# Performance work log

Measured on AMD Instinct MI355X. Metric: run time of the kernel, lower is better.

Reference implementation:

```python
import jax, jax.numpy as jnp
import numpy as np

V, D, H, F, L, SMAX = 32000, 768, 12, 3072, 6, 512
DN = D // H
NEG = -1e9
EPS = 1e-5


def _pos_encoding(S, d, dtype):
    # pe[pos,2i]   = sin(pos / 10000**(2i/d))
    # pe[pos,2i+1] = cos(pos / 10000**(2(i+1)/d))   (note the i+1, as in source)
    pos = jnp.arange(S, dtype=jnp.float32)[:, None]
    i = jnp.arange(d // 2, dtype=jnp.float32)[None, :]
    pe_sin = jnp.sin(pos / jnp.power(10000.0, 2.0 * i / d))
    pe_cos = jnp.cos(pos / jnp.power(10000.0, 2.0 * (i + 1.0) / d))
    pe = jnp.zeros((S, d), jnp.float32)
    pe = pe.at[:, 0::2].set(pe_sin).at[:, 1::2].set(pe_cos)
    return pe.astype(dtype)


def _layernorm(z, g, b):
    m = jnp.mean(z, axis=-1, keepdims=True)
    v = jnp.mean(jnp.square(z - m), axis=-1, keepdims=True)
    return (z - m) * jax.lax.rsqrt(v + EPS) * g + b


def setup_inputs() -> dict:
    key = jax.random.key(0)
    ks = jax.random.split(key, 20)
    s = 0.02
    inp = {
        "x": jax.random.randint(ks[0], (16, 512), 0, V, dtype=jnp.int64 if jax.config.read("jax_enable_x64") else jnp.int32),
        "padding_mask": jax.random.randint(ks[1], (16, 512, 512), 0, 2, dtype=jnp.int32),
        "emb": jax.random.normal(ks[2], (V, D), jnp.float32) * s,
        # per-head separate projections, stacked: [L, H, D, DN]
        "Wq": jax.random.normal(ks[3], (L, H, D, DN), jnp.float32) * s,
        "bq": jnp.zeros((L, H, DN), jnp.float32),
        "Wk": jax.random.normal(ks[4], (L, H, D, DN), jnp.float32) * s,
        "bk": jnp.zeros((L, H, DN), jnp.float32),
        "Wv": jax.random.normal(ks[5], (L, H, D, DN), jnp.float32) * s,
        "bv": jnp.zeros((L, H, DN), jnp.float32),
        "Wo": jax.random.normal(ks[6], (L, D, D), jnp.float32) * s,
        "bo": jnp.zeros((L, D), jnp.float32),
        "W1": jax.random.normal(ks[7], (L, D, F), jnp.float32) * s,
        "b1": jnp.zeros((L, F), jnp.float32),
        "W2": jax.random.normal(ks[8], (L, F, D), jnp.float32) * s,
        "b2": jnp.zeros((L, D), jnp.float32),
        "g1": jnp.ones((L, D), jnp.float32),
        "be1": jnp.zeros((L, D), jnp.float32),
        "g2": jnp.ones((L, D), jnp.float32),
        "be2": jnp.zeros((L, D), jnp.float32),
    }
    return inp


def reference(x, padding_mask, emb, Wq, bq, Wk, bk, Wv, bv, Wo, bo,
              W1, b1, W2, b2, g1, be1, g2, be2):
    B, S = x.shape
    h = emb[x]                                   # [B,S,D]
    h = h + _pos_encoding(S, D, h.dtype)[None]   # dropout is identity in eval
    bias = padding_mask.astype(h.dtype)[:, None] * NEG   # [B,1,S,S]
    scale = 1.0 / np.sqrt(DN)
    for l in range(L):
        q = jnp.einsum("bsd,hde->bhse", h, Wq[l]) + bq[l][None, :, None, :]
        k = jnp.einsum("bsd,hde->bhse", h, Wk[l]) + bk[l][None, :, None, :]
        v = jnp.einsum("bsd,hde->bhse", h, Wv[l]) + bv[l][None, :, None, :]
        scores = jnp.einsum("bhse,bhte->bhst", q, k) * scale + bias
        attn = jax.nn.softmax(scores, axis=-1)
        o = jnp.einsum("bhst,bhte->bhse", attn, v)        # [B,H,S,DN]
        o = o.transpose(0, 2, 1, 3).reshape(B, S, D)      # concat heads
        o = o @ Wo[l] + bo[l]
        h = _layernorm(h + o, g1[l], be1[l])
        ff = jax.nn.relu(h @ W1[l] + b1[l]) @ W2[l] + b2[l]
        h = _layernorm(h + ff, g2[l], be2[l])
    return h
```

## Files before the change

### kernel.cpp

```cpp
#include <hip/hip_runtime.h>
#include <hip/hip_bf16.h>
#include <math.h>

#define B_  16
#define S_  512
#define D_  768
#define H_  12
#define DN_ 64
#define F_  3072
#define L_  6
#define T_  (B_*S_)
#define QKVN 2304
#define TDC ((size_t)T_*D_)

typedef unsigned short ushort_t;
typedef short short8 __attribute__((ext_vector_type(8)));
typedef float floatx4 __attribute__((ext_vector_type(4)));

#define LDS_AS(p) ((__attribute__((address_space(3))) void*)(p))
#define GLB_AS(p) ((const __attribute__((address_space(1))) void*)(p))

static __device__ __forceinline__ float b2f(ushort_t u) {
  union { unsigned int i; float f; } x; x.i = ((unsigned int)u) << 16; return x.f;
}
static __device__ __forceinline__ ushort_t f2b(float f) {
  union { float f; unsigned int i; } x; x.f = f;
  unsigned int r = x.i + 0x7fffu + ((x.i >> 16) & 1u);
  return (ushort_t)(r >> 16);
}

__global__ __launch_bounds__(64) void probe_x(const int* __restrict__ x,
                                              int* __restrict__ xstride) {
  if (threadIdx.x == 0) {
    int allzero = 1;
    for (int i = 0; i < 64; ++i) allzero &= (x[2 * i + 1] == 0) ? 1 : 0;
    *xstride = allzero ? 2 : 1;
  }
}

__global__ __launch_bounds__(256) void pe_kernel(float* __restrict__ pe) {
  const int s = blockIdx.x;
  const float pos = (float)s;
  for (int d = threadIdx.x; d < D_; d += 256) {
    float v;
    if ((d & 1) == 0) {
      float freq = powf(10000.0f, -(float)d * (1.0f / 768.0f));
      v = sinf(pos * freq);
    } else {
      float freq = powf(10000.0f, -(float)(d + 1) * (1.0f / 768.0f));
      v = cosf(pos * freq);
    }
    pe[(size_t)s * D_ + d] = v;
  }
}

__global__ __launch_bounds__(256) void embed_pe(const int* __restrict__ x,
                                                const int* __restrict__ xstride,
                                                const float* __restrict__ emb,
                                                const float* __restrict__ pe,
                                                float* __restrict__ h32,
                                                ushort_t* __restrict__ h16) {
  const int t = blockIdx.x;
  const int s = t & (S_ - 1);
  const int tok = x[t * (*xstride)];
  const float* ep = emb + (size_t)tok * D_;
  const float* pp = pe + (size_t)s * D_;
  for (int d = threadIdx.x; d < D_; d += 256) {
    float v = ep[d] + pp[d];
    h32[(size_t)t * D_ + d] = v;
    h16[(size_t)t * D_ + d] = f2b(v);
  }
}

__global__ __launch_bounds__(256) void mask_bias(const int* __restrict__ mask,
                                                 ushort_t* __restrict__ bias) {
  const size_t i = ((size_t)blockIdx.x * 256 + threadIdx.x) * 4;
  int4 m = *(const int4*)(mask + i);
  ushort4 o;
  o.x = m.x ? f2b(-1e9f) : (ushort_t)0;
  o.y = m.y ? f2b(-1e9f) : (ushort_t)0;
  o.z = m.z ? f2b(-1e9f) : (ushort_t)0;
  o.w = m.w ? f2b(-1e9f) : (ushort_t)0;
  *(ushort4*)(bias + i) = o;
}

__global__ __launch_bounds__(256) void pack_bias(const float* __restrict__ bq,
                                                 const float* __restrict__ bk,
                                                 const float* __restrict__ bv,
                                                 float* __restrict__ bqkv) {
  const int i = blockIdx.x * 256 + threadIdx.x;
  if (i < L_ * D_) {
    const int l = i / D_, c = i - l * D_;
    bqkv[(size_t)l * QKVN + c]          = bq[i];
    bqkv[(size_t)l * QKVN + 768 + c]    = bk[i];
    bqkv[(size_t)l * QKVN + 1536 + c]   = bv[i];
  }
}

__global__ __launch_bounds__(256) void transpose_cast(const float* __restrict__ in,
                                                      ushort_t* __restrict__ out,
                                                      int R, int C, int ZH,
                                                      size_t strideL, size_t strideH) {
  __shared__ float tb[32][33];
  const int c0 = blockIdx.x * 32, r0 = blockIdx.y * 32;
  const int z = blockIdx.z;
  const float* ib = in + (size_t)z * R * C;
  ushort_t* ob = out + (size_t)(z / ZH) * strideL + (size_t)(z % ZH) * strideH;
  const int i = threadIdx.x >> 5;
  const int j = threadIdx.x & 31;
  #pragma unroll
  for (int t = 0; t < 4; ++t)
    tb[i + 8 * t][j] = ib[(size_t)(r0 + i + 8 * t) * C + c0 + j];
  __syncthreads();
  #pragma unroll
  for (int t = 0; t < 4; ++t)
    ob[(size_t)(c0 + i + 8 * t) * R + r0 + j] = f2b(tb[j][i + 8 * t]);
}

__global__ __launch_bounds__(256) void transpose_v(const ushort_t* __restrict__ qkv,
                                                   ushort_t* __restrict__ vT) {
  __shared__ ushort_t tb[32][33];
  const int s0 = blockIdx.x * 32, e0 = blockIdx.y * 32;
  const int bh = blockIdx.z;
  const int b = bh / 12, hh = bh - b * 12;
  const int i = threadIdx.x >> 5, j = threadIdx.x & 31;
  #pragma unroll
  for (int t = 0; t < 4; ++t)
    tb[i + 8 * t][j] = qkv[((size_t)(b * S_ + s0 + i + 8 * t)) * QKVN + 1536 + hh * 64 + e0 + j];
  __syncthreads();
  #pragma unroll
  for (int t = 0; t < 4; ++t)
    vT[((size_t)(bh * 64 + e0 + i + 8 * t)) * S_ + s0 + j] = tb[j][i + 8 * t];
}

template<int RELU>
__global__ __launch_bounds__(256) void gemm_mfma(const ushort_t* __restrict__ A,
                                                 const ushort_t* __restrict__ Bt,
                                                 const float* __restrict__ bias,
                                                 ushort_t* __restrict__ C,
                                                 int N, int K) {
  __shared__ ushort_t Alds[128 * 32];
  __shared__ ushort_t Blds[128 * 32];
  const int tid = threadIdx.x;
  const int lane = tid & 63, wave = tid >> 6;
  const int l16 = lane & 15, quad = lane >> 4;
  const int m0 = (wave >> 1) * 64, n0 = (wave & 1) * 64;
  const int nb = gridDim.x;
  const int flat = blockIdx.y * nb + blockIdx.x;
  const int grp = flat / (8 * nb);
  const int rem = flat - grp * 8 * nb;
  const int bm = (grp * 8 + (rem & 7)) * 128;
  const int bn = (rem >> 3) * 128;
  const int r0 = tid >> 2, koff = (tid & 3) * 8;

  const ushort_t* ga0 = A  + (size_t)(bm + r0) * K + koff;
  const ushort_t* ga1 = ga0 + (size_t)64 * K;
  const ushort_t* gb0 = Bt + (size_t)(bn + r0) * K + koff;
  const ushort_t* gb1 = gb0 + (size_t)64 * K;
  ushort_t* la0 = &Alds[tid * 8];
  ushort_t* la1 = &Alds[64 * 32 + tid * 8];
  ushort_t* lb0 = &Blds[tid * 8];
  ushort_t* lb1 = &Blds[64 * 32 + tid * 8];

  floatx4 acc[4][4] = {};
  for (int k0 = 0; k0 < K; k0 += 32) {
    __syncthreads();
    __builtin_amdgcn_global_load_lds(GLB_AS(ga0 + k0), LDS_AS(la0), 16, 0, 0);
    __builtin_amdgcn_global_load_lds(GLB_AS(ga1 + k0), LDS_AS(la1), 16, 0, 0);
    __builtin_amdgcn_global_load_lds(GLB_AS(gb0 + k0), LDS_AS(lb0), 16, 0, 0);
    __builtin_amdgcn_global_load_lds(GLB_AS(gb1 + k0), LDS_AS(lb1), 16, 0, 0);
    __syncthreads();
    short8 af[4], bf[4];
    #pragma unroll
    for (int fi = 0; fi < 4; ++fi)
      af[fi] = *(const short8*)&Alds[(m0 + fi * 16 + l16) * 32 + quad * 8];
    #pragma unroll
    for (int fj = 0; fj < 4; ++fj)
      bf[fj] = *(const short8*)&Blds[(n0 + fj * 16 + l16) * 32 + quad * 8];
    #pragma unroll
    for (int fi = 0; fi < 4; ++fi)
      #pragma unroll
      for (int fj = 0; fj < 4; ++fj)
        acc[fi][fj] = __builtin_amdgcn_mfma_f32_16x16x32_bf16(af[fi], bf[fj], acc[fi][fj], 0, 0, 0);
  }
  #pragma unroll
  for (int fi = 0; fi < 4; ++fi) {
    #pragma unroll
    for (int fj = 0; fj < 4; ++fj) {
      const int row = bm + m0 + fi * 16 + quad * 4;
      const int col = bn + n0 + fj * 16 + l16;
      const float bv = bias[col];
      #pragma unroll
      for (int r = 0; r < 4; ++r) {
        float v = acc[fi][fj][r] + bv;
        if (RELU) v = fmaxf(v, 0.0f);
        C[(size_t)(row + r) * N + col] = f2b(v);
      }
    }
  }
}

__global__ __launch_bounds__(256) void gemm_mfma_sk(const ushort_t* __restrict__ A,
                                                    const ushort_t* __restrict__ Bt,
                                                    const float* __restrict__ bias,
                                                    ushort_t* __restrict__ P,
                                                    int N, int K) {
  __shared__ ushort_t Alds[128 * 32];
  __shared__ ushort_t Blds[128 * 32];
  const int tid = threadIdx.x;
  const int lane = tid & 63, wave = tid >> 6;
  const int l16 = lane & 15, quad = lane >> 4;
  const int m0 = (wave >> 1) * 64, n0 = (wave & 1) * 64;
  const int nb = gridDim.x;
  const int flat = blockIdx.y * nb + blockIdx.x;
  const int grp = flat / (8 * nb);
  const int rem = flat - grp * 8 * nb;
  const int bm = (grp * 8 + (rem & 7)) * 128;
  const int bn = (rem >> 3) * 128;
  const int r0 = tid >> 2, koff = (tid & 3) * 8;
  const int z = blockIdx.z;
  const int Kh = K >> 1;

  const ushort_t* ga0 = A  + (size_t)(bm + r0) * K + (size_t)z * Kh + koff;
  const ushort_t* ga1 = ga0 + (size_t)64 * K;
  const ushort_t* gb0 = Bt + (size_t)(bn + r0) * K + (size_t)z * Kh + koff;
  const ushort_t* gb1 = gb0 + (size_t)64 * K;
  ushort_t* la0 = &Alds[tid * 8];
  ushort_t* la1 = &Alds[64 * 32 + tid * 8];
  ushort_t* lb0 = &Blds[tid * 8];
  ushort_t* lb1 = &Blds[64 * 32 + tid * 8];
  ushort_t* Pz = P + (size_t)z * T_ * N;

  floatx4 acc[4][4] = {};
  for (int k0 = 0; k0 < Kh; k0 += 32) {
    __syncthreads();
    __builtin_amdgcn_global_load_lds(GLB_AS(ga0 + k0), LDS_AS(la0), 16, 0, 0);
    __builtin_amdgcn_global_load_lds(GLB_AS(ga1 + k0), LDS_AS(la1), 16, 0, 0);
    __builtin_amdgcn_global_load_lds(GLB_AS(gb0 + k0), LDS_AS(lb0), 16, 0, 0);
    __builtin_amdgcn_global_load_lds(GLB_AS(gb1 + k0), LDS_AS(lb1), 16, 0, 0);
    __syncthreads();
    short8 af[4], bf[4];
    #pragma unroll
    for (int fi = 0; fi < 4; ++fi)
      af[fi] = *(const short8*)&Alds[(m0 + fi * 16 + l16) * 32 + quad * 8];
    #pragma unroll
    for (int fj = 0; fj < 4; ++fj)
      bf[fj] = *(const short8*)&Blds[(n0 + fj * 16 + l16) * 32 + quad * 8];
    #pragma unroll
    for (int fi = 0; fi < 4; ++fi)
      #pragma unroll
      for (int fj = 0; fj < 4; ++fj)
        acc[fi][fj] = __builtin_amdgcn_mfma_f32_16x16x32_bf16(af[fi], bf[fj], acc[fi][fj], 0, 0, 0);
  }
  #pragma unroll
  for (int fi = 0; fi < 4; ++fi) {
    #pragma unroll
    for (int fj = 0; fj < 4; ++fj) {
      const int row = bm + m0 + fi * 16 + quad * 4;
      const int col = bn + n0 + fj * 16 + l16;
      const float bv = (z == 0) ? bias[col] : 0.0f;
      #pragma unroll
      for (int r = 0; r < 4; ++r) {
        float v = acc[fi][fj][r] + bv;
        Pz[(size_t)(row + r) * N + col] = f2b(v);
      }
    }
  }
}

__global__ __launch_bounds__(256) void attn_mfma(const ushort_t* __restrict__ qkv,
                                                 const ushort_t* __restrict__ vT,
                                                 const ushort_t* __restrict__ bias,
                                                 ushort_t* __restrict__ o) {
  __shared__ ushort_t Qs[64][72];
  __shared__ ushort_t Ks[64][72];
  __shared__ ushort_t Vt[64][72];
  __shared__ ushort_t Ps[64][72];
  const int qt = blockIdx.x, hh = blockIdx.y, b = blockIdx.z;
  const int tid = threadIdx.x;
  const int lane = tid & 63, w = tid >> 6;
  const int l16 = lane & 15, quad = lane >> 4;

  for (int c = tid; c < 1024; c += 256) {
    const int row = c >> 4, e0 = (c & 15) * 4;
    *(ushort4*)&Qs[row][e0] =
        *(const ushort4*)(qkv + ((size_t)(b * S_ + qt * 64 + row)) * QKVN + hh * 64 + e0);
  }

  floatx4 Oa[4] = {};
  float mrow[4] = {-3e38f, -3e38f, -3e38f, -3e38f};
  float lrow[4] = {};
  const ushort_t* vbase = vT + ((size_t)(b * H_ + hh) * 64) * S_;

  for (int kt = 0; kt < 8; ++kt) {
    __syncthreads();
    for (int c = tid; c < 1024; c += 256) {
      const int row = c >> 4, e0 = (c & 15) * 4;
      *(ushort4*)&Ks[row][e0] =
          *(const ushort4*)(qkv + ((size_t)(b * S_ + kt * 64 + row)) * QKVN + 768 + hh * 64 + e0);
      *(ushort4*)&Vt[row][e0] =
          *(const ushort4*)(vbase + (size_t)row * S_ + kt * 64 + e0);
    }
    __syncthreads();

    floatx4 sa[4] = {};
    #pragma unroll
    for (int st = 0; st < 2; ++st) {
      short8 aq = *(const short8*)&Qs[w * 16 + l16][st * 32 + quad * 8];
      #pragma unroll
      for (int fj = 0; fj < 4; ++fj) {
        short8 bk = *(const short8*)&Ks[fj * 16 + l16][st * 32 + quad * 8];
        sa[fj] = __builtin_amdgcn_mfma_f32_16x16x32_bf16(aq, bk, sa[fj], 0, 0, 0);
      }
    }

    #pragma unroll
    for (int r = 0; r < 4; ++r) {
      const int qrow = qt * 64 + w * 16 + quad * 4 + r;
      const ushort_t* bp = bias + ((size_t)b * S_ + qrow) * S_ + kt * 64 + l16;
      float s0 = sa[0][r] * 0.125f + b2f(bp[0]);
      float s1 = sa[1][r] * 0.125f + b2f(bp[16]);
      float s2 = sa[2][r] * 0.125f + b2f(bp[32]);
      float s3 = sa[3][r] * 0.125f + b2f(bp[48]);
      float mt = fmaxf(fmaxf(s0, s1), fmaxf(s2, s3));
      mt = fmaxf(mt, __shfl_xor(mt, 1)); mt = fmaxf(mt, __shfl_xor(mt, 2));
      mt = fmaxf(mt, __shfl_xor(mt, 4)); mt = fmaxf(mt, __shfl_xor(mt, 8));
      const float mn = fmaxf(mrow[r], mt);
      const float alpha = __expf(mrow[r] - mn);
      mrow[r] = mn;
      float p0 = __expf(s0 - mn), p1 = __expf(s1 - mn);
      float p2 = __expf(s2 - mn), p3 = __expf(s3 - mn);
      const int prow = w * 16 + quad * 4 + r;
      Ps[prow][ 0 + l16] = f2b(p0);
      Ps[prow][16 + l16] = f2b(p1);
      Ps[prow][32 + l16] = f2b(p2);
      Ps[prow][48 + l16] = f2b(p3);
      float rs = p0 + p1 + p2 + p3;
      rs += __shfl_xor(rs, 1); rs += __shfl_xor(rs, 2);
      rs += __shfl_xor(rs, 4); rs += __shfl_xor(rs, 8);
      lrow[r] = lrow[r] * alpha + rs;
      Oa[0][r] *= alpha; Oa[1][r] *= alpha; Oa[2][r] *= alpha; Oa[3][r] *= alpha;
    }

    #pragma unroll
    for (int st = 0; st < 2; ++st) {
      short8 ap = *(const short8*)&Ps[w * 16 + l16][st * 32 + quad * 8];
      #pragma unroll
      for (int fe = 0; fe < 4; ++fe) {
        short8 bv = *(const short8*)&Vt[fe * 16 + l16][st * 32 + quad * 8];
        Oa[fe] = __builtin_amdgcn_mfma_f32_16x16x32_bf16(ap, bv, Oa[fe], 0, 0, 0);
      }
    }
  }

  #pragma unroll
  for (int r = 0; r < 4; ++r) {
    const float inv = 1.0f / lrow[r];
    const size_t tok = (size_t)(b * S_ + qt * 64 + w * 16 + quad * 4 + r);
    #pragma unroll
    for (int fe = 0; fe < 4; ++fe)
      o[tok * D_ + hh * 64 + fe * 16 + l16] = f2b(Oa[fe][r] * inv);
  }
}

__global__ __launch_bounds__(256) void add_ln(float* __restrict__ h,
                                              const ushort_t* __restrict__ r,
                                              const float* __restrict__ g,
                                              const float* __restrict__ be,
                                              ushort_t* __restrict__ h16) {
  const int t = blockIdx.x;
  const int tid = threadIdx.x;
  __shared__ float red[8];
  const size_t base = (size_t)t * D_;
  float x0 = h[base + tid]       + b2f(r[base + tid])       + b2f(r[TDC + base + tid]);
  float x1 = h[base + tid + 256] + b2f(r[base + tid + 256]) + b2f(r[TDC + base + tid + 256]);
  float x2 = h[base + tid + 512] + b2f(r[base + tid + 512]) + b2f(r[TDC + base + tid + 512]);
  float s = x0 + x1 + x2;
  #pragma unroll
  for (int off = 32; off > 0; off >>= 1) s += __shfl_down(s, off);
  if ((tid & 63) == 0) red[tid >> 6] = s;
  __syncthreads();
  if (tid == 0) red[4] = (red[0] + red[1] + red[2] + red[3]) * (1.0f / 768.0f);
  __syncthreads();
  const float m = red[4];
  float d0 = x0 - m, d1 = x1 - m, d2 = x2 - m;
  float s2 = d0 * d0 + d1 * d1 + d2 * d2;
  #pragma unroll
  for (int off = 32; off > 0; off >>= 1) s2 += __shfl_down(s2, off);
  if ((tid & 63) == 0) red[tid >> 6] = s2;
  __syncthreads();
  if (tid == 0) red[5] = (red[0] + red[1] + red[2] + red[3]) * (1.0f / 768.0f);
  __syncthreads();
  const float rs = rsqrtf(red[5] + 1e-5f);
  float y0 = d0 * rs * g[tid]       + be[tid];
  float y1 = d1 * rs * g[tid + 256] + be[tid + 256];
  float y2 = d2 * rs * g[tid + 512] + be[tid + 512];
  h[base + tid]       = y0; h16[base + tid]       = f2b(y0);
  h[base + tid + 256] = y1; h16[base + tid + 256] = f2b(y1);
  h[base + tid + 512] = y2; h16[base + tid + 512] = f2b(y2);
}

__global__ __launch_bounds__(256) void write_out(const float* __restrict__ h,
                                                 float* __restrict__ out, int n) {
  int i = blockIdx.x * 256 + threadIdx.x;
  if (i < n) out[i] = h[i];
}

extern "C" void kernel_launch(void* const* d_in, const int* in_sizes, int n_in,
                              void* d_out, int out_size, void* d_ws, size_t ws_size,
                              hipStream_t stream) {
  (void)in_sizes; (void)n_in; (void)out_size; (void)ws_size;
  const int* x    = (const int*)d_in[0];
  const int* mask = (const int*)d_in[1];
  const float* emb = (const float*)d_in[2];
  const float* Wq  = (const float*)d_in[3];
  const float* bq  = (const float*)d_in[4];
  const float* Wk  = (const float*)d_in[5];
  const float* bk  = (const float*)d_in[6];
  const float* Wv  = (const float*)d_in[7];
  const float* bv  = (const float*)d_in[8];
  const float* Wo  = (const float*)d_in[9];
  const float* bo  = (const float*)d_in[10];
  const float* W1  = (const float*)d_in[11];
  const float* b1  = (const float*)d_in[12];
  const float* W2  = (const float*)d_in[13];
  const float* b2  = (const float*)d_in[14];
  const float* g1  = (const float*)d_in[15];
  const float* be1 = (const float*)d_in[16];
  const float* g2  = (const float*)d_in[17];
  const float* be2 = (const float*)d_in[18];

  const size_t TD  = TDC;
  const size_t DD  = (size_t)D_ * D_;
  const size_t WDD = (size_t)L_ * DD;
  const size_t WDF = (size_t)L_ * D_ * F_;

  float* h32 = (float*)d_ws;
  ushort_t* h16  = (ushort_t*)(h32 + TD);
  ushort_t* qkv16 = h16 + TD;
  ushort_t* o1   = qkv16 + 3 * TD;
  ushort_t* o2   = o1 + TD;
  ushort_t* ff   = qkv16;
  ushort_t* vT   = o2 + TD;
  ushort_t* bias16 = vT + TD;
  ushort_t* WqkvT = bias16 + (size_t)B_ * S_ * S_;
  ushort_t* WoT  = WqkvT + 3 * WDD;
  ushort_t* W1T  = WoT + WDD;
  ushort_t* W2T  = W1T + WDF;
  float* bqkv    = (float*)(W2T + WDF);
  int* xstride   = (int*)(bqkv + (size_t)L_ * QKVN);
  float* pe32    = (float*)o1;

  probe_x<<<dim3(1), 64, 0, stream>>>(x, xstride);
  pe_kernel<<<dim3(S_), 256, 0, stream>>>(pe32);
  transpose_cast<<<dim3(2, 24, 72), 256, 0, stream>>>(Wq, WqkvT,          768, 64, 12, 3 * DD, (size_t)64 * 768);
  transpose_cast<<<dim3(2, 24, 72), 256, 0, stream>>>(Wk, WqkvT + DD,     768, 64, 12, 3 * DD, (size_t)64 * 768);
  transpose_cast<<<dim3(2, 24, 72), 256, 0, stream>>>(Wv, WqkvT + 2 * DD, 768, 64, 12, 3 * DD, (size_t)64 * 768);
  transpose_cast<<<dim3(24, 24, 6), 256, 0, stream>>>(Wo, WoT, 768, 768, 1, DD, 0);
  transpose_cast<<<dim3(96, 24, 6), 256, 0, stream>>>(W1, W1T, 768, 3072, 1, (size_t)D_ * F_, 0);
  transpose_cast<<<dim3(24, 96, 6), 256, 0, stream>>>(W2, W2T, 3072, 768, 1, (size_t)D_ * F_, 0);
  pack_bias<<<dim3((L_ * D_ + 255) / 256), 256, 0, stream>>>(bq, bk, bv, bqkv);
  mask_bias<<<dim3((B_ * S_ * S_) / 1024), 256, 0, stream>>>(mask, bias16);
  embed_pe<<<dim3(T_), 256, 0, stream>>>(x, xstride, emb, pe32, h32, h16);

  const dim3 gQKV(QKVN / 128, T_ / 128);
  const dim3 gDsk(D_ / 128, T_ / 128, 2);
  const dim3 gF(F_ / 128, T_ / 128);
  for (int l = 0; l < L_; ++l) {
    const size_t oDD = (size_t)l * DD;
    const size_t oDF = (size_t)l * D_ * F_;
    gemm_mfma<0><<<gQKV, 256, 0, stream>>>(h16, WqkvT + (size_t)l * 3 * DD, bqkv + (size_t)l * QKVN, qkv16, QKVN, D_);
    transpose_v<<<dim3(16, 2, B_ * H_), 256, 0, stream>>>(qkv16, vT);
    attn_mfma<<<dim3(8, H_, B_), 256, 0, stream>>>(qkv16, vT, bias16, o1);
    gemm_mfma_sk<<<gDsk, 256, 0, stream>>>(o1, WoT + oDD, bo + l * D_, o2, D_, D_);
    add_ln<<<dim3(T_), 256, 0, stream>>>(h32, o2, g1 + l * D_, be1 + l * D_, h16);
    gemm_mfma<1><<<gF, 256, 0, stream>>>(h16, W1T + oDF, b1 + l * F_, ff, F_, D_);
    gemm_mfma_sk<<<gDsk, 256, 0, stream>>>(ff, W2T + oDF, b2 + l * D_, o2, D_, F_);
    add_ln<<<dim3(T_), 256, 0, stream>>>(h32, o2, g2 + l * D_, be2 + l * D_, h16);
  }
  write_out<<<dim3((unsigned)(TD / 256)), 256, 0, stream>>>(h32, (float*)d_out, (int)TD);
}
```

Measured before the change: 1.998 ms.

## Pack padding mask into bitmask and remap attention grid for XCD locality

Replaces the bf16 additive bias tensor (8 MB per pass) with a one-bit-per-key mask built by a ballot kernel, so each attention row reads one 64-bit word per key tile instead of 64 bf16 values. The attention launch becomes a flat 1-D grid whose index is decoded so that all query tiles of a given batch-head land on the same XCD, aiming to improve L2 reuse of K and V. It adds bit-extract arithmetic per score, and the mapping assumes the hardware assigns blocks to XCDs round-robin.

Result: no change. 1.987 ms (-0.6%).

```diff
diff --git a/kernel.cpp b/kernel.cpp
--- a/kernel.cpp
+++ b/kernel.cpp
@@ -72,16 +72,13 @@
   }
 }
 
-__global__ __launch_bounds__(256) void mask_bias(const int* __restrict__ mask,
-                                                 ushort_t* __restrict__ bias) {
-  const size_t i = ((size_t)blockIdx.x * 256 + threadIdx.x) * 4;
-  int4 m = *(const int4*)(mask + i);
-  ushort4 o;
-  o.x = m.x ? f2b(-1e9f) : (ushort_t)0;
-  o.y = m.y ? f2b(-1e9f) : (ushort_t)0;
-  o.z = m.z ? f2b(-1e9f) : (ushort_t)0;
-  o.w = m.w ? f2b(-1e9f) : (ushort_t)0;
-  *(ushort4*)(bias + i) = o;
+__global__ __launch_bounds__(256) void mask_bits(const int* __restrict__ mask,
+                                                 unsigned long long* __restrict__ bits) {
+  const int gw = (blockIdx.x * 256 + threadIdx.x) >> 6;
+  const int lane = threadIdx.x & 63;
+  const int m = mask[(size_t)gw * 64 + lane];
+  unsigned long long bal = __ballot(m != 0);
+  if (lane == 0) bits[gw] = bal;
 }
 
 __global__ __launch_bounds__(256) void pack_bias(const float* __restrict__ bq,
@@ -270,13 +267,19 @@
 
 __global__ __launch_bounds__(256) void attn_mfma(const ushort_t* __restrict__ qkv,
                                                  const ushort_t* __restrict__ vT,
-                                                 const ushort_t* __restrict__ bias,
+                                                 const unsigned long long* __restrict__ mbits,
                                                  ushort_t* __restrict__ o) {
   __shared__ ushort_t Qs[64][72];
   __shared__ ushort_t Ks[64][72];
   __shared__ ushort_t Vt[64][72];
   __shared__ ushort_t Ps[64][72];
-  const int qt = blockIdx.x, hh = blockIdx.y, b = blockIdx.z;
+  const int F = blockIdx.x;
+  const int xcd = F & 7;
+  const int sfl = F >> 3;
+  const int qt = sfl & 7;
+  const int gg = sfl >> 3;
+  const int bh = gg * 8 + xcd;
+  const int b = bh / 12, hh = bh - b * 12;
   const int tid = threadIdx.x;
   const int lane = tid & 63, w = tid >> 6;
   const int l16 = lane & 15, quad = lane >> 4;
@@ -317,11 +320,11 @@
     #pragma unroll
     for (int r = 0; r < 4; ++r) {
       const int qrow = qt * 64 + w * 16 + quad * 4 + r;
-      const ushort_t* bp = bias + ((size_t)b * S_ + qrow) * S_ + kt * 64 + l16;
-      float s0 = sa[0][r] * 0.125f + b2f(bp[0]);
-      float s1 = sa[1][r] * 0.125f + b2f(bp[16]);
-      float s2 = sa[2][r] * 0.125f + b2f(bp[32]);
-      float s3 = sa[3][r] * 0.125f + b2f(bp[48]);
+      const unsigned long long m64 = mbits[((size_t)(b * S_ + qrow) << 3) + kt];
+      float s0 = sa[0][r] * 0.125f + (((m64 >> l16) & 1ull)        ? -1e9f : 0.0f);
+      float s1 = sa[1][r] * 0.125f + (((m64 >> (16 + l16)) & 1ull) ? -1e9f : 0.0f);
+      float s2 = sa[2][r] * 0.125f + (((m64 >> (32 + l16)) & 1ull) ? -1e9f : 0.0f);
+      float s3 = sa[3][r] * 0.125f + (((m64 >> (48 + l16)) & 1ull) ? -1e9f : 0.0f);
       float mt = fmaxf(fmaxf(s0, s1), fmaxf(s2, s3));
       mt = fmaxf(mt, __shfl_xor(mt, 1)); mt = fmaxf(mt, __shfl_xor(mt, 2));
       mt = fmaxf(mt, __shfl_xor(mt, 4)); mt = fmaxf(mt, __shfl_xor(mt, 8));
@@ -450,6 +453,7 @@
   float* bqkv    = (float*)(W2T + WDF);
   int* xstride   = (int*)(bqkv + (size_t)L_ * QKVN);
   float* pe32    = (float*)o1;
+  unsigned long long* mbits = (unsigned long long*)bias16;
 
   probe_x<<<dim3(1), 64, 0, stream>>>(x, xstride);
   pe_kernel<<<dim3(S_), 256, 0, stream>>>(pe32);
@@ -460,7 +464,7 @@
   transpose_cast<<<dim3(96, 24, 6), 256, 0, stream>>>(W1, W1T, 768, 3072, 1, (size_t)D_ * F_, 0);
   transpose_cast<<<dim3(24, 96, 6), 256, 0, stream>>>(W2, W2T, 3072, 768, 1, (size_t)D_ * F_, 0);
   pack_bias<<<dim3((L_ * D_ + 255) / 256), 256, 0, stream>>>(bq, bk, bv, bqkv);
-  mask_bias<<<dim3((B_ * S_ * S_) / 1024), 256, 0, stream>>>(mask, bias16);
+  mask_bits<<<dim3((B_ * S_ * S_) / 256), 256, 0, stream>>>(mask, mbits);
   embed_pe<<<dim3(T_), 256, 0, stream>>>(x, xstride, emb, pe32, h32, h16);
 
   const dim3 gQKV(QKVN / 128, T_ / 128);
@@ -471,7 +475,7 @@
     const size_t oDF = (size_t)l * D_ * F_;
     gemm_mfma<0><<<gQKV, 256, 0, stream>>>(h16, WqkvT + (size_t)l * 3 * DD, bqkv + (size_t)l * QKVN, qkv16, QKVN, D_);
     transpose_v<<<dim3(16, 2, B_ * H_), 256, 0, stream>>>(qkv16, vT);
-    attn_mfma<<<dim3(8, H_, B_), 256, 0, stream>>>(qkv16, vT, bias16, o1);
+    attn_mfma<<<dim3(8 * H_ * B_), 256, 0, stream>>>(qkv16, vT, mbits, o1);
     gemm_mfma_sk<<<gDsk, 256, 0, stream>>>(o1, WoT + oDD, bo + l * D_, o2, D_, D_);
     add_ln<<<dim3(T_), 256, 0, stream>>>(h32, o2, g1 + l * D_, be1 + l * D_, h16);
     gemm_mfma<1><<<gF, 256, 0, stream>>>(h16, W1T + oDF, b1 + l * F_, ff, F_, D_);
```
